# Kernel tuning notes

Measured on AMD Instinct MI355X. Metric: run time of the kernel, lower is better.

The kernel has to match this reference:

```python
import jax, jax.numpy as jnp
import numpy as np

N, E, F_IN, H, D, C = 50000, 800000, 128, 4, 64, 40
HD = H * D
NEG_SLOPE = 0.2


def setup_inputs() -> dict:
    key = jax.random.key(0)
    ks = jax.random.split(key, 16)
    x = jax.random.normal(ks[0], (N, F_IN), dtype=jnp.float32)
    edge_index = jax.random.randint(ks[1], (2, E), 0, N, dtype=jnp.int64)
    def glorot(k, shape):
        fan = shape[0] + shape[-1]
        return jax.random.normal(k, shape, dtype=jnp.float32) * jnp.sqrt(2.0 / fan)
    params = {
        'W1': glorot(ks[2], (F_IN, HD)), 'as1': glorot(ks[3], (H, D)), 'ad1': glorot(ks[4], (H, D)), 'b1': jnp.zeros((HD,), jnp.float32),
        'W2': glorot(ks[5], (HD, HD)),   'as2': glorot(ks[6], (H, D)), 'ad2': glorot(ks[7], (H, D)), 'b2': jnp.zeros((HD,), jnp.float32),
        'W3': glorot(ks[8], (HD, HD)),   'as3': glorot(ks[9], (H, D)), 'ad3': glorot(ks[10], (H, D)), 'b3': jnp.zeros((HD,), jnp.float32),
        'Wl': glorot(ks[11], (HD, C)),   'bl': jnp.zeros((C,), jnp.float32),
    }
    return {'x': x, 'edge_index': edge_index, **params}


def gat_layer(x, src, dst, W, a_src, a_dst, b):
    # x: [N, F] -> h: [N, H, D]
    h = (x @ W).reshape(N, H, D)
    alpha_s = jnp.sum(h * a_src, axis=-1)  # [N, H]
    alpha_d = jnp.sum(h * a_dst, axis=-1)  # [N, H]
    e = alpha_s[src] + alpha_d[dst]        # [E', H]
    e = jnp.where(e > 0, e, NEG_SLOPE * e)  # leaky_relu
    # segment softmax over destination nodes
    m = jax.ops.segment_max(e, dst, num_segments=N)  # [N, H]
    m = jnp.where(jnp.isfinite(m), m, 0.0)
    ex = jnp.exp(e - m[dst])
    s = jax.ops.segment_sum(ex, dst, num_segments=N)  # [N, H]
    att = ex / (s[dst] + 1e-16)                        # [E', H]
    # weighted scatter-aggregate of source features
    out = jax.ops.segment_sum(h[src] * att[:, :, None], dst, num_segments=N)  # [N, H, D]
    return out.reshape(N, HD) + b


def reference(x, edge_index, W1, as1, ad1, b1, W2, as2, ad2, b2, W3, as3, ad3, b3, Wl, bl):
    # PyG GATConv adds self-loops by default
    loops = jnp.arange(N, dtype=edge_index.dtype)
    src = jnp.concatenate([edge_index[0], loops])
    dst = jnp.concatenate([edge_index[1], loops])
    # dropout is identity in eval mode
    h = jax.nn.elu(gat_layer(x, src, dst, W1, as1, ad1, b1))
    h = jax.nn.elu(gat_layer(h, src, dst, W2, as2, ad2, b2))
    h = jax.nn.elu(gat_layer(h, src, dst, W3, as3, ad3, b3))
    logits = h @ Wl + bl
    return jax.nn.log_softmax(logits, axis=1)
```

## Files before the change

### kernel.cpp

```cpp
#include <hip/hip_runtime.h>
#include <math.h>

#define NN 50000
#define NE 800000
#define ET (NE + NN)
#define FIN 128
#define HDIM 256
#define NHEAD 4
#define NCLS 40
#define NEG 0.2f
#define NB_SCAN ((NN + 255) / 256)

typedef short bf16x8 __attribute__((ext_vector_type(8)));
typedef float f32x4 __attribute__((ext_vector_type(4)));

__device__ __forceinline__ unsigned short f2b(float f) {
    unsigned int u = __float_as_uint(f);
    unsigned int r = (u + 0x7fffu + ((u >> 16) & 1u)) >> 16;
    return (unsigned short)r;
}
__device__ __forceinline__ unsigned int cvtpk(float lo, float hi) {
    unsigned int r;
    asm volatile("v_cvt_pk_bf16_f32 %0, %1, %2" : "=v"(r) : "v"(lo), "v"(hi));
    return r;
}
__device__ __forceinline__ float b2f(unsigned short u) {
    unsigned int x = ((unsigned int)u) << 16;
    return __uint_as_float(x);
}

#define GLOAD_LDS16(gp, lp)                                                     \
    __builtin_amdgcn_global_load_lds(                                           \
        (const __attribute__((address_space(1))) void*)(gp),                    \
        (__attribute__((address_space(3))) void*)(lp), 16, 0, 0)

__global__ void detect_kernel(const int* __restrict__ ei32, int* __restrict__ flag) {
    int lane = threadIdx.x;
    int nz = ei32[1 + 2 * lane] | ei32[129 + 2 * lane];
    unsigned long long b = __ballot(nz != 0);
    if (lane == 0) *flag = (b == 0ull) ? 1 : 0;
}

__device__ __forceinline__ int load_node(const int* ei32, int is64, long long idx) {
    return is64 ? ei32[2 * idx] : ei32[idx];
}

__global__ void deg_kernel(const int* __restrict__ ei32, const int* __restrict__ flag,
                           int* __restrict__ deg) {
    int e = blockIdx.x * blockDim.x + threadIdx.x;
    if (e >= ET) return;
    int is64 = *flag;
    int d = (e < NE) ? load_node(ei32, is64, (long long)NE + e) : (e - NE);
    atomicAdd(&deg[d], 1);
}

__global__ void scan1(const int* __restrict__ deg, int* __restrict__ incl,
                      int* __restrict__ bsum) {
    __shared__ int sm[256];
    int i = blockIdx.x * 256 + threadIdx.x;
    int v = (i < NN) ? deg[i] : 0;
    sm[threadIdx.x] = v;
    __syncthreads();
    for (int o = 1; o < 256; o <<= 1) {
        int add = (threadIdx.x >= o) ? sm[threadIdx.x - o] : 0;
        __syncthreads();
        sm[threadIdx.x] += add;
        __syncthreads();
    }
    if (i < NN) incl[i] = sm[threadIdx.x];
    if (threadIdx.x == 255) bsum[blockIdx.x] = sm[255];
}

__global__ void scan2(int* __restrict__ bsum) {
    __shared__ int sm[256];
    int t = threadIdx.x;
    sm[t] = (t < NB_SCAN) ? bsum[t] : 0;
    __syncthreads();
    if (t == 0) {
        int run = 0;
        for (int b = 0; b < NB_SCAN; b++) { int v = sm[b]; sm[b] = run; run += v; }
    }
    __syncthreads();
    if (t < NB_SCAN) bsum[t] = sm[t];
}

__global__ void scan3(const int* __restrict__ incl, const int* __restrict__ bsum,
                      const int* __restrict__ deg, int* __restrict__ indptr,
                      int* __restrict__ cursor) {
    int i = blockIdx.x * 256 + threadIdx.x;
    if (i < NN) {
        int v = bsum[blockIdx.x] + incl[i];
        indptr[i + 1] = v;
        cursor[i] = v - deg[i];
    }
    if (i == 0) indptr[0] = 0;
}

__global__ void fill_kernel(const int* __restrict__ ei32, const int* __restrict__ flag,
                            int* __restrict__ cursor, int* __restrict__ esrc) {
    int e = blockIdx.x * blockDim.x + threadIdx.x;
    if (e >= ET) return;
    int is64 = *flag;
    int s, d;
    if (e < NE) {
        s = load_node(ei32, is64, (long long)e);
        d = load_node(ei32, is64, (long long)NE + e);
    } else {
        s = d = e - NE;
    }
    int pos = atomicAdd(&cursor[d], 1);
    esrc[pos] = s;
}

__global__ __launch_bounds__(256) void conv_kernel(const float* __restrict__ in,
                                                   unsigned short* __restrict__ out, int n) {
    int i = (blockIdx.x * 256 + threadIdx.x) * 8;
    if (i + 8 > n) return;
    float4 f0 = *(const float4*)(in + i);
    float4 f1 = *(const float4*)(in + i + 4);
    uint4 pk;
    pk.x = cvtpk(f0.x, f0.y);
    pk.y = cvtpk(f0.z, f0.w);
    pk.z = cvtpk(f1.x, f1.y);
    pk.w = cvtpk(f1.z, f1.w);
    *(uint4*)(out + i) = pk;
}

__global__ __launch_bounds__(256) void wconv3_kernel(const float* __restrict__ W1,
                                                     const float* __restrict__ W2,
                                                     const float* __restrict__ W3,
                                                     unsigned short* __restrict__ Wt1,
                                                     unsigned short* __restrict__ Wt2,
                                                     unsigned short* __restrict__ Wt3) {
    __shared__ float sm[32][33];
    int z = blockIdx.z;
    const float* W = (z == 0) ? W1 : (z == 1) ? W2 : W3;
    unsigned short* Wt = (z == 0) ? Wt1 : (z == 1) ? Wt2 : Wt3;
    int K = (z == 0) ? FIN : HDIM;
    int k0 = blockIdx.y * 32;
    if (k0 >= K) return;
    int tx = threadIdx.x & 31, ty = threadIdx.x >> 5;
    int n0 = blockIdx.x * 32;
#pragma unroll
    for (int j = 0; j < 4; j++)
        sm[ty + j * 8][tx] = W[(size_t)(k0 + ty + j * 8) * HDIM + n0 + tx];
    __syncthreads();
#pragma unroll
    for (int j = 0; j < 4; j++)
        Wt[(size_t)(n0 + ty + j * 8) * K + k0 + tx] = f2b(sm[tx][ty + j * 8]);
}

__global__ __launch_bounds__(256) void gemm_mfma(const unsigned short* __restrict__ A,
                                                 const unsigned short* __restrict__ Bt,
                                                 unsigned short* __restrict__ Cb,
                                                 const float* __restrict__ a_s,
                                                 const float* __restrict__ a_d,
                                                 float* __restrict__ als,
                                                 float* __restrict__ ald,
                                                 int M, int K) {
    __shared__ unsigned short smem[12288];
    int bid = blockIdx.x;
    int xcd = bid & 7, g = bid >> 3;
    int cblk = g & 3, rg = g >> 2;
    int rblk = rg * 8 + xcd;
    int r0 = rblk * 128, n0 = cblk * 64;
    if (r0 >= M) return;

    int t = threadIdx.x;
    int lane = t & 63, wid = t >> 6;

    f32x4 acc[2][4];
#pragma unroll
    for (int m = 0; m < 2; m++)
#pragma unroll
        for (int n = 0; n < 4; n++)
            acc[m][n] = (f32x4){0.f, 0.f, 0.f, 0.f};

    int fr = lane & 15;
    int kg = lane >> 4;

    int aslot[4], arow[4], apl[4];
#pragma unroll
    for (int c = 0; c < 4; c++) {
        aslot[c] = wid * 256 + c * 64 + lane;
        apl[c] = aslot[c] >> 7;
        int r = r0 + (aslot[c] & 127);
        arow[c] = (r > M - 1) ? (M - 1) : r;
    }
    int bslot[2], bcol[2], bpl[2];
#pragma unroll
    for (int c = 0; c < 2; c++) {
        bslot[c] = 1024 + wid * 128 + c * 64 + lane;
        int s = bslot[c] - 1024;
        bpl[c] = s >> 6;
        bcol[c] = n0 + (s & 63);
    }

    for (int k0 = 0; k0 < K; k0 += 64) {
#pragma unroll
        for (int c = 0; c < 4; c++)
            GLOAD_LDS16(A + (size_t)arow[c] * K + k0 + apl[c] * 8, smem + (size_t)aslot[c] * 8);
#pragma unroll
        for (int c = 0; c < 2; c++)
            GLOAD_LDS16(Bt + (size_t)bcol[c] * K + k0 + bpl[c] * 8, smem + (size_t)bslot[c] * 8);
        __syncthreads();
#pragma unroll
        for (int kk = 0; kk < 64; kk += 32) {
            int pl = (kk >> 3) + kg;
            bf16x8 a[2], b[4];
#pragma unroll
            for (int m = 0; m < 2; m++)
                a[m] = *(const bf16x8*)(smem + ((pl << 7) + wid * 32 + m * 16 + fr) * 8);
#pragma unroll
            for (int n = 0; n < 4; n++)
                b[n] = *(const bf16x8*)(smem + (1024 + (pl << 6) + n * 16 + fr) * 8);
#pragma unroll
            for (int m = 0; m < 2; m++)
#pragma unroll
                for (int n = 0; n < 4; n++)
                    acc[m][n] = __builtin_amdgcn_mfma_f32_16x16x32_bf16(a[m], b[n], acc[m][n], 0, 0, 0);
        }
        __syncthreads();
    }

    int rbase = r0 + wid * 32 + kg * 4;
    int cbase = n0 + fr;
    int head = n0 >> 6;
    float asv[4], adv[4];
#pragma unroll
    for (int n = 0; n < 4; n++) {
        asv[n] = a_s[cbase + n * 16];
        adv[n] = a_d[cbase + n * 16];
    }
#pragma unroll
    for (int m = 0; m < 2; m++)
#pragma unroll
        for (int q = 0; q < 4; q++) {
            int gr = rbase + m * 16 + q;
            float vs = 0.f, vd = 0.f;
#pragma unroll
            for (int n = 0; n < 4; n++) {
                float v = acc[m][n][q];
                vs += v * asv[n];
                vd += v * adv[n];
            }
#pragma unroll
            for (int o = 8; o > 0; o >>= 1) {
                vs += __shfl_xor(vs, o);
                vd += __shfl_xor(vd, o);
            }
            if (fr == 0 && gr < M) {
                als[gr * NHEAD + head] = vs;
                ald[gr * NHEAD + head] = vd;
            }
        }

    unsigned short (*Cs)[68] = (unsigned short(*)[68])&smem[0];
    int lr0 = wid * 32 + kg * 4;
#pragma unroll
    for (int m = 0; m < 2; m++)
#pragma unroll
        for (int q = 0; q < 4; q++)
#pragma unroll
            for (int n = 0; n < 4; n++)
                Cs[lr0 + m * 16 + q][fr + n * 16] = f2b(acc[m][n][q]);
    __syncthreads();
    int tr = t >> 4;
    int tc = (t & 15) * 4;
#pragma unroll
    for (int rr = 0; rr < 8; rr++) {
        int lr = tr + rr * 16;
        int gr = r0 + lr;
        if (gr < M) *(ushort4*)(Cb + (size_t)gr * HDIM + n0 + tc) = *(const ushort4*)&Cs[lr][tc];
    }
}

__global__ __launch_bounds__(256) void agg_kernel(const unsigned short* __restrict__ projb,
                                                  const float* __restrict__ als,
                                                  const float* __restrict__ ald,
                                                  const int* __restrict__ indptr,
                                                  const int* __restrict__ esrc,
                                                  const float* __restrict__ bias,
                                                  unsigned short* __restrict__ featb) {
    int wid = threadIdx.x >> 6;
    int v = blockIdx.x * 4 + wid;
    if (v >= NN) return;
    int lane = threadIdx.x & 63;
    int h = lane >> 4;
    int sub = lane & 15;
    int beg = indptr[v], end = indptr[v + 1];
    float adv = ald[v * NHEAD + h];

    float e0 = 0.f, e1 = 0.f;
    int s0r = 0, s1r = 0;
    float m = -INFINITY, ss = 0.f;
    int idx = 0;
    for (int i = beg + sub; i < end; i += 16, idx++) {
        int s = esrc[i];
        float e = als[s * NHEAD + h] + adv;
        e = e > 0.f ? e : NEG * e;
        if (idx == 0) { e0 = e; s0r = s; }
        else if (idx == 1) { e1 = e; s1r = s; }
        if (e > m) {
            ss = ss * __expf(m - e) + 1.f;
            m = e;
        } else {
            ss += __expf(e - m);
        }
    }
#pragma unroll
    for (int o = 8; o > 0; o >>= 1) {
        float m2 = __shfl_xor(m, o);
        float s2 = __shfl_xor(ss, o);
        float mn = fmaxf(m, m2);
        float a = (m == mn) ? ss : ss * __expf(m - mn);
        float b = (m2 == mn) ? s2 : s2 * __expf(m2 - mn);
        m = mn;
        ss = a + b;
    }
    float inv = 1.f / (ss + 1e-16f);

    float4 acc = make_float4(0.f, 0.f, 0.f, 0.f);
    int chunk = 0;
    for (int c = beg; c < end; c += 16, chunk++) {
        int rem = end - c;
        int sreg;
        float eC;
        if (chunk == 0) { sreg = s0r; eC = e0; }
        else if (chunk == 1) { sreg = s1r; eC = e1; }
        else {
            int i = c + (sub < rem ? sub : rem - 1);
            sreg = esrc[i];
            eC = als[sreg * NHEAD + h] + adv;
            eC = eC > 0.f ? eC : NEG * eC;
        }
        float wreg = (sub < rem) ? __expf(eC - m) * inv : 0.f;

        ushort4 p[16];
#pragma unroll
        for (int j = 0; j < 16; j++) {
            int s = __shfl(sreg, j);
            p[j] = *(const ushort4*)(projb + (size_t)s * HDIM + (lane << 2));
        }
#pragma unroll
        for (int j = 0; j < 16; j++) {
            float w = __shfl(wreg, (h << 4) | j);
            acc.x += b2f(p[j].x) * w;
            acc.y += b2f(p[j].y) * w;
            acc.z += b2f(p[j].z) * w;
            acc.w += b2f(p[j].w) * w;
        }
    }

    const float4 b4 = *(const float4*)(bias + (lane << 2));
    float4 r;
    r.x = acc.x + b4.x;
    r.y = acc.y + b4.y;
    r.z = acc.z + b4.z;
    r.w = acc.w + b4.w;
    r.x = r.x > 0.f ? r.x : __expf(r.x) - 1.f;
    r.y = r.y > 0.f ? r.y : __expf(r.y) - 1.f;
    r.z = r.z > 0.f ? r.z : __expf(r.z) - 1.f;
    r.w = r.w > 0.f ? r.w : __expf(r.w) - 1.f;
    uint2 o2;
    o2.x = cvtpk(r.x, r.y);
    o2.y = cvtpk(r.z, r.w);
    *(uint2*)(featb + (size_t)v * HDIM + (lane << 2)) = o2;
}

__global__ __launch_bounds__(256) void final_kernel(const unsigned short* __restrict__ featb,
                                                    const float* __restrict__ Wl,
                                                    const float* __restrict__ bl,
                                                    float* __restrict__ out) {
    const int BK = 16;
    __shared__ float As[BK][65];
    __shared__ float Bs[BK][65];
    int tx = threadIdx.x & 15, ty = threadIdx.x >> 4;
    int row0 = blockIdx.x * 64;
    float acc[4][4] = {};
    for (int k0 = 0; k0 < HDIM; k0 += BK) {
#pragma unroll
        for (int i = 0; i < 4; i++) {
            int l = threadIdx.x + 256 * i;
            int r = l >> 4, c = l & 15;
            int gr = row0 + r;
            float v = 0.f;
            if (gr < NN) v = b2f(featb[(size_t)gr * HDIM + k0 + c]);
            As[c][r] = v;
        }
#pragma unroll
        for (int i = 0; i < 4; i++) {
            int l = threadIdx.x + 256 * i;
            int r = l >> 6, c = l & 63;
            Bs[r][c] = (c < NCLS) ? Wl[(size_t)(k0 + r) * NCLS + c] : 0.f;
        }
        __syncthreads();
#pragma unroll
        for (int k = 0; k < BK; k++) {
            float a[4], b[4];
#pragma unroll
            for (int i = 0; i < 4; i++) a[i] = As[k][ty + 16 * i];
#pragma unroll
            for (int j = 0; j < 4; j++) b[j] = Bs[k][tx + 16 * j];
#pragma unroll
            for (int i = 0; i < 4; i++)
#pragma unroll
                for (int j = 0; j < 4; j++) acc[i][j] += a[i] * b[j];
        }
        __syncthreads();
    }
    float b0 = bl[tx], b1 = bl[tx + 16], b2 = (tx < 8) ? bl[tx + 32] : 0.f;
#pragma unroll
    for (int i = 0; i < 4; i++) {
        int gr = row0 + ty + 16 * i;
        if (gr >= NN) continue;
        float l0 = acc[i][0] + b0;
        float l1 = acc[i][1] + b1;
        float l2 = (tx < 8) ? acc[i][2] + b2 : -INFINITY;
        float m = fmaxf(fmaxf(l0, l1), l2);
#pragma unroll
        for (int o = 8; o > 0; o >>= 1) m = fmaxf(m, __shfl_xor(m, o));
        float s = __expf(l0 - m) + __expf(l1 - m) + ((tx < 8) ? __expf(l2 - m) : 0.f);
#pragma unroll
        for (int o = 8; o > 0; o >>= 1) s += __shfl_xor(s, o);
        float lse = m + __logf(s);
        out[(size_t)gr * NCLS + tx] = l0 - lse;
        out[(size_t)gr * NCLS + tx + 16] = l1 - lse;
        if (tx < 8) out[(size_t)gr * NCLS + tx + 32] = l2 - lse;
    }
}

extern "C" void kernel_launch(void* const* d_in, const int* in_sizes, int n_in,
                              void* d_out, int out_size, void* d_ws, size_t ws_size,
                              hipStream_t stream) {
    const float* x  = (const float*)d_in[0];
    const int* ei32 = (const int*)d_in[1];
    const float* W1 = (const float*)d_in[2];
    const float* as1 = (const float*)d_in[3];
    const float* ad1 = (const float*)d_in[4];
    const float* b1 = (const float*)d_in[5];
    const float* W2 = (const float*)d_in[6];
    const float* as2 = (const float*)d_in[7];
    const float* ad2 = (const float*)d_in[8];
    const float* b2 = (const float*)d_in[9];
    const float* W3 = (const float*)d_in[10];
    const float* as3 = (const float*)d_in[11];
    const float* ad3 = (const float*)d_in[12];
    const float* b3 = (const float*)d_in[13];
    const float* Wl = (const float*)d_in[14];
    const float* bl = (const float*)d_in[15];
    float* out = (float*)d_out;

    char* w = (char*)d_ws;
    unsigned short* projb = (unsigned short*)w;  w += (size_t)NN * HDIM * 2;
    unsigned short* featb = (unsigned short*)w;  w += (size_t)NN * HDIM * 2;
    unsigned short* xb    = (unsigned short*)w;  w += (size_t)NN * FIN * 2;
    unsigned short* Wt1b  = (unsigned short*)w;  w += (size_t)HDIM * FIN * 2;
    unsigned short* Wt2b  = (unsigned short*)w;  w += (size_t)HDIM * HDIM * 2;
    unsigned short* Wt3b  = (unsigned short*)w;  w += (size_t)HDIM * HDIM * 2;
    float* als  = (float*)w;  w += (size_t)NN * NHEAD * 4;
    float* ald  = (float*)w;  w += (size_t)NN * NHEAD * 4;
    int* deg    = (int*)w;    w += (size_t)NN * 4;
    int* incl   = (int*)w;    w += (size_t)NN * 4;
    int* bsum   = (int*)w;    w += 256 * 4;
    int* indptr = (int*)w;    w += (size_t)(NN + 1) * 4;
    int* cursor = (int*)w;    w += (size_t)NN * 4;
    int* esrc   = (int*)w;    w += (size_t)ET * 4;
    int* flag   = (int*)w;    w += 64;

    conv_kernel<<<(NN * FIN / 8 + 255) / 256, 256, 0, stream>>>(x, xb, NN * FIN);
    wconv3_kernel<<<dim3(8, 8, 3), 256, 0, stream>>>(W1, W2, W3, Wt1b, Wt2b, Wt3b);

    hipMemsetAsync(deg, 0, (size_t)NN * 4, stream);
    detect_kernel<<<1, 64, 0, stream>>>(ei32, flag);
    deg_kernel<<<(ET + 255) / 256, 256, 0, stream>>>(ei32, flag, deg);
    scan1<<<NB_SCAN, 256, 0, stream>>>(deg, incl, bsum);
    scan2<<<1, 256, 0, stream>>>(bsum);
    scan3<<<NB_SCAN, 256, 0, stream>>>(incl, bsum, deg, indptr, cursor);
    fill_kernel<<<(ET + 255) / 256, 256, 0, stream>>>(ei32, flag, cursor, esrc);

    int ggrid = 8 * 4 * (((NN + 127) / 128 + 7) / 8);
    int agrid = (NN + 3) / 4;

    gemm_mfma<<<ggrid, 256, 0, stream>>>(xb, Wt1b, projb, as1, ad1, als, ald, NN, FIN);
    agg_kernel<<<agrid, 256, 0, stream>>>(projb, als, ald, indptr, esrc, b1, featb);
    gemm_mfma<<<ggrid, 256, 0, stream>>>(featb, Wt2b, projb, as2, ad2, als, ald, NN, HDIM);
    agg_kernel<<<agrid, 256, 0, stream>>>(projb, als, ald, indptr, esrc, b2, featb);
    gemm_mfma<<<ggrid, 256, 0, stream>>>(featb, Wt3b, projb, as3, ad3, als, ald, NN, HDIM);
    agg_kernel<<<agrid, 256, 0, stream>>>(projb, als, ald, indptr, esrc, b3, featb);
    final_kernel<<<(NN + 63) / 64, 256, 0, stream>>>(featb, Wl, bl, out);
}
```

Baseline: 428.3 us.

## Double-buffer GEMM LDS tiles with swizzle and fold int64 detect into kernels

The MFMA GEMM now double-buffers its LDS tiles. It issues the global-to-LDS loads for the next k-tile before computing on the current one, and uses explicit vmcnt waits with raw barriers in place of two syncthreads per iteration. It also applies a row-rotation swizzle to the LDS slot mapping to reduce bank conflicts on the fragment reads. Separately, the standalone int64-detect kernel is removed and each block of the degree and fill kernels sniffs the index width itself, saving one launch at the cost of redundant per-block loads. LDS use doubles, which may reduce occupancy.

```diff
diff --git a/kernel.cpp b/kernel.cpp
--- a/kernel.cpp
+++ b/kernel.cpp
@@ -34,22 +34,25 @@
         (const __attribute__((address_space(1))) void*)(gp),                    \
         (__attribute__((address_space(3))) void*)(lp), 16, 0, 0)
 
-__global__ void detect_kernel(const int* __restrict__ ei32, int* __restrict__ flag) {
-    int lane = threadIdx.x;
-    int nz = ei32[1 + 2 * lane] | ei32[129 + 2 * lane];
-    unsigned long long b = __ballot(nz != 0);
-    if (lane == 0) *flag = (b == 0ull) ? 1 : 0;
+__device__ __forceinline__ int sniff_is64(const int* __restrict__ ei32, int* s64p) {
+    if (threadIdx.x < 64) {
+        int nz = ei32[1 + 2 * threadIdx.x] | ei32[129 + 2 * threadIdx.x];
+        unsigned long long b = __ballot(nz != 0);
+        if (threadIdx.x == 0) *s64p = (b == 0ull) ? 1 : 0;
+    }
+    __syncthreads();
+    return *s64p;
 }
 
 __device__ __forceinline__ int load_node(const int* ei32, int is64, long long idx) {
     return is64 ? ei32[2 * idx] : ei32[idx];
 }
 
-__global__ void deg_kernel(const int* __restrict__ ei32, const int* __restrict__ flag,
-                           int* __restrict__ deg) {
+__global__ void deg_kernel(const int* __restrict__ ei32, int* __restrict__ deg) {
+    __shared__ int s64;
+    int is64 = sniff_is64(ei32, &s64);
     int e = blockIdx.x * blockDim.x + threadIdx.x;
     if (e >= ET) return;
-    int is64 = *flag;
     int d = (e < NE) ? load_node(ei32, is64, (long long)NE + e) : (e - NE);
     atomicAdd(&deg[d], 1);
 }
@@ -96,11 +99,12 @@
     if (i == 0) indptr[0] = 0;
 }
 
-__global__ void fill_kernel(const int* __restrict__ ei32, const int* __restrict__ flag,
+__global__ void fill_kernel(const int* __restrict__ ei32,
                             int* __restrict__ cursor, int* __restrict__ esrc) {
+    __shared__ int s64;
+    int is64 = sniff_is64(ei32, &s64);
     int e = blockIdx.x * blockDim.x + threadIdx.x;
     if (e >= ET) return;
-    int is64 = *flag;
     int s, d;
     if (e < NE) {
         s = load_node(ei32, is64, (long long)e);
@@ -158,7 +162,7 @@
                                                  float* __restrict__ als,
                                                  float* __restrict__ ald,
                                                  int M, int K) {
-    __shared__ unsigned short smem[12288];
+    __shared__ unsigned short smem[2 * 1536 * 8];
     int bid = blockIdx.x;
     int xcd = bid & 7, g = bid >> 3;
     int cblk = g & 3, rg = g >> 2;
@@ -168,6 +172,8 @@
 
     int t = threadIdx.x;
     int lane = t & 63, wid = t >> 6;
+    int fr = lane & 15;
+    int kg = lane >> 4;
 
     f32x4 acc[2][4];
 #pragma unroll
@@ -175,17 +181,15 @@
 #pragma unroll
         for (int n = 0; n < 4; n++)
             acc[m][n] = (f32x4){0.f, 0.f, 0.f, 0.f};
-
-    int fr = lane & 15;
-    int kg = lane >> 4;
 
     int aslot[4], arow[4], apl[4];
 #pragma unroll
     for (int c = 0; c < 4; c++) {
         aslot[c] = wid * 256 + c * 64 + lane;
         apl[c] = aslot[c] >> 7;
-        int r = r0 + (aslot[c] & 127);
-        arow[c] = (r > M - 1) ? (M - 1) : r;
+        int r = ((aslot[c] & 127) - 2 * apl[c]) & 127;
+        int grow = r0 + r;
+        arow[c] = (grow > M - 1) ? (M - 1) : grow;
     }
     int bslot[2], bcol[2], bpl[2];
 #pragma unroll
@@ -193,35 +197,53 @@
         bslot[c] = 1024 + wid * 128 + c * 64 + lane;
         int s = bslot[c] - 1024;
         bpl[c] = s >> 6;
-        bcol[c] = n0 + (s & 63);
-    }
-
-    for (int k0 = 0; k0 < K; k0 += 64) {
-#pragma unroll
-        for (int c = 0; c < 4; c++)
-            GLOAD_LDS16(A + (size_t)arow[c] * K + k0 + apl[c] * 8, smem + (size_t)aslot[c] * 8);
-#pragma unroll
-        for (int c = 0; c < 2; c++)
-            GLOAD_LDS16(Bt + (size_t)bcol[c] * K + k0 + bpl[c] * 8, smem + (size_t)bslot[c] * 8);
-        __syncthreads();
+        bcol[c] = n0 + (((s & 63) - 2 * bpl[c]) & 63);
+    }
+
+#define STAGE(dbase, koff)                                                      \
+    do {                                                                        \
+        _Pragma("unroll")                                                       \
+        for (int c = 0; c < 4; c++)                                             \
+            GLOAD_LDS16(A + (size_t)arow[c] * K + (koff) + apl[c] * 8,          \
+                        smem + (size_t)((dbase) + aslot[c]) * 8);               \
+        _Pragma("unroll")                                                       \
+        for (int c = 0; c < 2; c++)                                             \
+            GLOAD_LDS16(Bt + (size_t)bcol[c] * K + (koff) + bpl[c] * 8,         \
+                        smem + (size_t)((dbase) + bslot[c]) * 8);               \
+    } while (0)
+
+    STAGE(0, 0);
+    int nt = K >> 6;
+    for (int tt = 0; tt < nt; ++tt) {
+        int cur = (tt & 1) ? 1536 : 0;
+        if (tt + 1 < nt) {
+            STAGE(cur ^ 1536, (tt + 1) * 64);
+            asm volatile("s_waitcnt vmcnt(6)" ::: "memory");
+        } else {
+            asm volatile("s_waitcnt vmcnt(0)" ::: "memory");
+        }
+        __builtin_amdgcn_s_barrier();
 #pragma unroll
         for (int kk = 0; kk < 64; kk += 32) {
             int pl = (kk >> 3) + kg;
             bf16x8 a[2], b[4];
 #pragma unroll
             for (int m = 0; m < 2; m++)
-                a[m] = *(const bf16x8*)(smem + ((pl << 7) + wid * 32 + m * 16 + fr) * 8);
+                a[m] = *(const bf16x8*)(smem +
+                    (size_t)(cur + (pl << 7) + ((wid * 32 + m * 16 + fr + 2 * pl) & 127)) * 8);
 #pragma unroll
             for (int n = 0; n < 4; n++)
-                b[n] = *(const bf16x8*)(smem + (1024 + (pl << 6) + n * 16 + fr) * 8);
+                b[n] = *(const bf16x8*)(smem +
+                    (size_t)(cur + 1024 + (pl << 6) + ((n * 16 + fr + 2 * pl) & 63)) * 8);
 #pragma unroll
             for (int m = 0; m < 2; m++)
 #pragma unroll
                 for (int n = 0; n < 4; n++)
                     acc[m][n] = __builtin_amdgcn_mfma_f32_16x16x32_bf16(a[m], b[n], acc[m][n], 0, 0, 0);
         }
-        __syncthreads();
-    }
+        __builtin_amdgcn_s_barrier();
+    }
+#undef STAGE
 
     int rbase = r0 + wid * 32 + kg * 4;
     int cbase = n0 + fr;
@@ -466,18 +488,16 @@
     int* indptr = (int*)w;    w += (size_t)(NN + 1) * 4;
     int* cursor = (int*)w;    w += (size_t)NN * 4;
     int* esrc   = (int*)w;    w += (size_t)ET * 4;
-    int* flag   = (int*)w;    w += 64;
 
     conv_kernel<<<(NN * FIN / 8 + 255) / 256, 256, 0, stream>>>(x, xb, NN * FIN);
     wconv3_kernel<<<dim3(8, 8, 3), 256, 0, stream>>>(W1, W2, W3, Wt1b, Wt2b, Wt3b);
 
     hipMemsetAsync(deg, 0, (size_t)NN * 4, stream);
-    detect_kernel<<<1, 64, 0, stream>>>(ei32, flag);
-    deg_kernel<<<(ET + 255) / 256, 256, 0, stream>>>(ei32, flag, deg);
+    deg_kernel<<<(ET + 255) / 256, 256, 0, stream>>>(ei32, deg);
     scan1<<<NB_SCAN, 256, 0, stream>>>(deg, incl, bsum);
     scan2<<<1, 256, 0, stream>>>(bsum);
     scan3<<<NB_SCAN, 256, 0, stream>>>(incl, bsum, deg, indptr, cursor);
-    fill_kernel<<<(ET + 255) / 256, 256, 0, stream>>>(ei32, flag, cursor, esrc);
+    fill_kernel<<<(ET + 255) / 256, 256, 0, stream>>>(ei32, cursor, esrc);
 
     int ggrid = 8 * 4 * (((NN + 127) / 128 + 7) / 8);
     int agrid = (NN + 3) / 4;
```

New measurement: 425.6 us. Within noise of the previous version (-0.6%).
